# Optimization experiments

Hardware: AMD Instinct MI355X
Metric: run time of the kernel (lower is better)

Reference implementation:

```python
import jax, jax.numpy as jnp
import numpy as np

B, T, D, H = 4, 2048, 1024, 16
DH = D // H  # 64
EPS = 1e-5


def _layernorm(x, g, b):
    mu = jnp.mean(x, axis=-1, keepdims=True)
    var = jnp.var(x, axis=-1, keepdims=True)
    return (x - mu) * jax.lax.rsqrt(var + EPS) * g + b


def setup_inputs() -> dict:
    key = jax.random.key(0)
    ks = jax.random.split(key, 12)
    s = 0.02
    x = jax.random.normal(ks[0], (B, T, D), dtype=jnp.float32)
    # causal mask (the repo registers tril as the eos_mask buffer)
    eos_mask = jnp.broadcast_to(jnp.tril(jnp.ones((T, T), dtype=jnp.int32)), (B, T, T))
    Wq = jax.random.normal(ks[1], (H, D, DH), dtype=jnp.float32) * s
    Wk = jax.random.normal(ks[2], (H, D, DH), dtype=jnp.float32) * s
    Wv = jax.random.normal(ks[3], (H, D, DH), dtype=jnp.float32) * s
    Wp = jax.random.normal(ks[4], (D, D), dtype=jnp.float32) * s
    bp = jnp.zeros((D,), dtype=jnp.float32)
    W1 = jax.random.normal(ks[5], (D, 4 * D), dtype=jnp.float32) * s
    b1 = jnp.zeros((4 * D,), dtype=jnp.float32)
    W2 = jax.random.normal(ks[6], (4 * D, D), dtype=jnp.float32) * s
    b2 = jnp.zeros((D,), dtype=jnp.float32)
    g1 = jnp.ones((D,), dtype=jnp.float32)
    beta1 = jnp.zeros((D,), dtype=jnp.float32)
    g2 = jnp.ones((D,), dtype=jnp.float32)
    beta2 = jnp.zeros((D,), dtype=jnp.float32)
    return dict(x=x, eos_mask=eos_mask, Wq=Wq, Wk=Wk, Wv=Wv, Wp=Wp, bp=bp,
                W1=W1, b1=b1, W2=W2, b2=b2, g1=g1, beta1=beta1, g2=g2, beta2=beta2)


def reference(x, eos_mask, Wq, Wk, Wv, Wp, bp, W1, b1, W2, b2, g1, beta1, g2, beta2):
    # x: [B,T,D]; eos_mask: [B,T,T]
    x1 = _layernorm(x, g1, beta1)
    q = jnp.einsum('btd,hdk->bhtk', x1, Wq)
    k = jnp.einsum('btd,hdk->bhtk', x1, Wk)
    v = jnp.einsum('btd,hdk->bhtk', x1, Wv)
    # NOTE: original scales by 1/sqrt(C) where C = d_model (not d_head)
    scores = jnp.einsum('bhtk,bhsk->bhts', q, k) / np.sqrt(x.shape[-1]).astype(np.float32)
    scores = jnp.where(eos_mask[:, None, :, :] == 0, jnp.float32(-jnp.inf), scores)
    wei = jax.nn.softmax(scores, axis=-1)
    attn = jnp.einsum('bhts,bhsk->bhtk', wei, v)          # [B,H,T,DH]
    attn = attn.transpose(0, 2, 1, 3).reshape(x.shape)    # concat heads -> [B,T,D]
    attn = attn @ Wp + bp
    x2 = x1 + attn
    x3 = _layernorm(x2, g2, beta2)
    mlp = jax.nn.relu(x3 @ W1 + b1) @ W2 + b2
    out = x3 + mlp
    return out
```

## Files before the change

kernel.cpp:

```cpp
#include <hip/hip_runtime.h>


#define B_ 4
#define T_ 2048
#define D_ 1024
#define H_ 16
#define DH_ 64

using u16 = unsigned short;
typedef short bf16x8 __attribute__((ext_vector_type(8)));
typedef float f32x4 __attribute__((ext_vector_type(4)));

#define GLOAD_LDS16(g, l)                                                          \
  __builtin_amdgcn_global_load_lds((const __attribute__((address_space(1))) void*)(g), \
                                   (__attribute__((address_space(3))) void*)(l), 16, 0, 0)

#define CVTPK(d, lo, hi) asm("v_cvt_pk_bf16_f32 %0, %1, %2" : "=v"(d) : "v"(lo), "v"(hi))
#define BARSB() do { __builtin_amdgcn_s_barrier(); __builtin_amdgcn_sched_barrier(0); } while (0)

__device__ __forceinline__ f32x4 mfma16(bf16x8 a, bf16x8 b, f32x4 c) {
  return __builtin_amdgcn_mfma_f32_16x16x32_bf16(a, b, c, 0, 0, 0);
}

__device__ __forceinline__ u16 f2bf(float f) {
  union { float f; unsigned u; } v; v.f = f;
  unsigned r = v.u + 0x7fffu + ((v.u >> 16) & 1u);
  return (u16)(r >> 16);
}
__device__ __forceinline__ float bf2f(u16 h) {
  union { unsigned u; float f; } v; v.u = ((unsigned)h) << 16; return v.f;
}

template<typename TI>
__global__ __launch_bounds__(256)
void ln_kernel(const TI* __restrict__ x, const float* __restrict__ g,
               const float* __restrict__ be, u16* __restrict__ yb)
{
  const int row = blockIdx.x;
  const int tid = threadIdx.x;
  float v0, v1, v2, v3;
  if constexpr (sizeof(TI) == 4) {
    const float4 vx = ((const float4*)(x + (size_t)row * D_))[tid];
    v0 = vx.x; v1 = vx.y; v2 = vx.z; v3 = vx.w;
  } else {
    const ushort4 vx = ((const ushort4*)((const u16*)x + (size_t)row * D_))[tid];
    v0 = bf2f(vx.x); v1 = bf2f(vx.y); v2 = bf2f(vx.z); v3 = bf2f(vx.w);
  }
  float s  = v0 + v1 + v2 + v3;
  float s2 = v0*v0 + v1*v1 + v2*v2 + v3*v3;
#pragma unroll
  for (int m = 1; m < 64; m <<= 1) { s += __shfl_xor(s, m); s2 += __shfl_xor(s2, m); }
  __shared__ float red[8];
  const int w = tid >> 6;
  if ((tid & 63) == 0) { red[w] = s; red[4 + w] = s2; }
  __syncthreads();
  s  = red[0] + red[1] + red[2] + red[3];
  s2 = red[4] + red[5] + red[6] + red[7];
  const float mu   = s * (1.0f / D_);
  const float rstd = rsqrtf(s2 * (1.0f / D_) - mu * mu + 1e-5f);
  const float4 gg = ((const float4*)g)[tid];
  const float4 bb = ((const float4*)be)[tid];
  ushort4 pk;
  pk.x = f2bf((v0 - mu) * rstd * gg.x + bb.x);
  pk.y = f2bf((v1 - mu) * rstd * gg.y + bb.y);
  pk.z = f2bf((v2 - mu) * rstd * gg.z + bb.z);
  pk.w = f2bf((v3 - mu) * rstd * gg.w + bb.w);
  ((ushort4*)(yb + (size_t)row * D_))[tid] = pk;
}

__global__ __launch_bounds__(256)
void transpose_cvt(const float* __restrict__ in, u16* __restrict__ out, int R, int C)
{
  __shared__ float tile[32][33];
  const int c0 = blockIdx.x * 32, r0 = blockIdx.y * 32;
  const float* ip = in + (size_t)blockIdx.z * R * C;
  u16* op = out + (size_t)blockIdx.z * R * C;
  const int tx = threadIdx.x, ty = threadIdx.y;
#pragma unroll
  for (int j = 0; j < 4; ++j)
    tile[ty + j * 8][tx] = ip[(size_t)(r0 + ty + j * 8) * C + (c0 + tx)];
  __syncthreads();
#pragma unroll
  for (int j = 0; j < 4; ++j)
    op[(size_t)(c0 + ty + j * 8) * R + (r0 + tx)] = f2bf(tile[tx][ty + j * 8]);
}

__global__ __launch_bounds__(256)
void transpose_bf(const u16* __restrict__ in, u16* __restrict__ out, int R, int C)
{
  __shared__ u16 tile[32][34];
  const int c0 = blockIdx.x * 32, r0 = blockIdx.y * 32;
  const u16* ip = in + (size_t)blockIdx.z * R * C;
  u16* op = out + (size_t)blockIdx.z * R * C;
  const int tx = threadIdx.x, ty = threadIdx.y;
#pragma unroll
  for (int j = 0; j < 4; ++j)
    tile[ty + j * 8][tx] = ip[(size_t)(r0 + ty + j * 8) * C + (c0 + tx)];
  __syncthreads();
#pragma unroll
  for (int j = 0; j < 4; ++j)
    op[(size_t)(c0 + ty + j * 8) * R + (r0 + tx)] = tile[tx][ty + j * 8];
}

#define MODE_QKV 0
#define MODE_WP 1
#define MODE_MLP1 2
#define MODE_MLP2 3

template<int MODE>
__global__ __launch_bounds__(512, 2)
void gemm256v3(const u16* __restrict__ A, const u16* __restrict__ Bt,
               int M, int N, int K,
               const float* __restrict__ bias, const u16* __restrict__ resid,
               float* __restrict__ outf, u16* __restrict__ outb,
               u16* __restrict__ qo, u16* __restrict__ ko, u16* __restrict__ vo)
{
  __shared__ __align__(16) u16 Ash[2][256 * 64];
  __shared__ __align__(16) u16 Bsh[2][256 * 64];
  const int t = threadIdx.x, w = t >> 6, l = t & 63, lg = l >> 4, lr = l & 15;
  const int wr = w >> 2, wc = w & 3;

  const int gx = gridDim.x;
  const int nwg = gx * gridDim.y;
  const int bid = blockIdx.y * gx + blockIdx.x;
  const int cpx = nwg >> 3;
  const int virt = (bid & 7) * cpx + (bid >> 3);
  const int bn0 = (virt % gx) * 256, bm0 = (virt / gx) * 256;

  f32x4 acc[8][4] = {};

  const int srow = t >> 3;
  const int sc16 = (t & 7) ^ (srow & 7);
  const u16* gAs = A  + (size_t)(bm0 + srow) * K + sc16 * 8;
  const u16* gBs = Bt + (size_t)(bn0 + srow) * K + sc16 * 8;

#define ISS2_A(R, BUF, ko) GLOAD_LDS16(gAs + (size_t)(R) * 64 * K + (ko), &Ash[BUF][(R) * 4096 + w * 512])
#define ISS2_B(R, BUF, ko) GLOAD_LDS16(gBs + (size_t)(R) * 64 * K + (ko), &Bsh[BUF][(R) * 4096 + w * 512])

  const int nkt = K >> 6;
  ISS2_A(0, 0, 0); ISS2_A(1, 0, 0); ISS2_A(2, 0, 0); ISS2_A(3, 0, 0);
  ISS2_B(0, 0, 0); ISS2_B(1, 0, 0); ISS2_B(2, 0, 0); ISS2_B(3, 0, 0);
  if (nkt > 1) {
    ISS2_A(0, 1, 64); ISS2_A(2, 1, 64);
    asm volatile("s_waitcnt vmcnt(2)" ::: "memory");
  } else {
    asm volatile("s_waitcnt vmcnt(0)" ::: "memory");
  }
  BARSB();

  auto rdA0k = [&](int buf, int m) -> bf16x8 {
    const int r = wr * 128 + m * 16 + lr;
    return *(const bf16x8*)((const char*)&Ash[buf][0] + r * 128 + (((0 + lg) ^ (r & 7)) << 4));
  };
  auto rdA1k = [&](int buf, int m) -> bf16x8 {
    const int r = wr * 128 + m * 16 + lr;
    return *(const bf16x8*)((const char*)&Ash[buf][0] + r * 128 + (((4 + lg) ^ (r & 7)) << 4));
  };
  auto rdB0k = [&](int buf, int n) -> bf16x8 {
    const int r = wc * 64 + n * 16 + lr;
    return *(const bf16x8*)((const char*)&Bsh[buf][0] + r * 128 + (((0 + lg) ^ (r & 7)) << 4));
  };
  auto rdB1k = [&](int buf, int n) -> bf16x8 {
    const int r = wc * 64 + n * 16 + lr;
    return *(const bf16x8*)((const char*)&Bsh[buf][0] + r * 128 + (((4 + lg) ^ (r & 7)) << 4));
  };

  bf16x8 afr[4][2], bfr[4][2];

  for (int i = 0; i < nkt; ++i) {
    const int buf = i & 1, nb = buf ^ 1;
    const size_t k1 = (size_t)(i + 1) << 6, k2 = (size_t)(i + 2) << 6;
    const bool n1 = (i + 1 < nkt), n2 = (i + 2 < nkt);

#pragma unroll
    for (int m = 0; m < 4; ++m) { afr[m][0] = rdA0k(buf, m); afr[m][1] = rdA1k(buf, m); }
#pragma unroll
    for (int n = 0; n < 4; ++n) { bfr[n][0] = rdB0k(buf, n); bfr[n][1] = rdB1k(buf, n); }
    if (n1) { ISS2_A(1, nb, k1); ISS2_A(3, nb, k1); ISS2_B(2, nb, k1); ISS2_B(3, nb, k1); }
    __builtin_amdgcn_s_setprio(1);
#pragma unroll
    for (int m = 0; m < 4; ++m)
#pragma unroll
      for (int n = 0; n < 4; ++n) {
        acc[m][n] = mfma16(afr[m][0], bfr[n][0], acc[m][n]);
        acc[m][n] = mfma16(afr[m][1], bfr[n][1], acc[m][n]);
      }
    __builtin_amdgcn_s_setprio(0);
    BARSB();

#pragma unroll
    for (int m = 0; m < 4; ++m) { afr[m][0] = rdA0k(buf, 4 + m); afr[m][1] = rdA1k(buf, 4 + m); }
    if (n1) { ISS2_B(0, nb, k1); ISS2_B(1, nb, k1); }
    if (n2) { ISS2_A(0, buf, k2); ISS2_A(2, buf, k2); }
    __builtin_amdgcn_s_setprio(1);
#pragma unroll
    for (int m = 0; m < 4; ++m)
#pragma unroll
      for (int n = 0; n < 4; ++n) {
        acc[4 + m][n] = mfma16(afr[m][0], bfr[n][0], acc[4 + m][n]);
        acc[4 + m][n] = mfma16(afr[m][1], bfr[n][1], acc[4 + m][n]);
      }
    __builtin_amdgcn_s_setprio(0);
    if (n1) {
      if (n2) asm volatile("s_waitcnt vmcnt(2)" ::: "memory");
      else    asm volatile("s_waitcnt vmcnt(0)" ::: "memory");
      BARSB();
    }
  }
#undef ISS2_A
#undef ISS2_B

#pragma unroll
  for (int m = 0; m < 8; ++m) {
#pragma unroll
    for (int n = 0; n < 4; ++n) {
#pragma unroll
      for (int r = 0; r < 4; ++r) {
        const int row = bm0 + wr * 128 + m * 16 + lg * 4 + r;
        const int col = bn0 + wc * 64 + n * 16 + lr;
        float v = acc[m][n][r];
        if constexpr (MODE == MODE_QKV) {
          const int sel = col >> 10, hh = (col >> 6) & 15, dh = col & 63;
          const int bi = row >> 11, tt = row & 2047;
          u16* dst = (sel == 0) ? qo : (sel == 1) ? ko : vo;
          dst[(((size_t)bi * H_ + hh) * T_ + tt) * DH_ + dh] = f2bf(v);
        } else if constexpr (MODE == MODE_MLP1) {
          v += bias[col];
          outb[(size_t)row * N + col] = f2bf(v > 0.f ? v : 0.f);
        }
      }
    }
  }
}

template<int MODE>
__global__ __launch_bounds__(512, 4)
void gemm128(const u16* __restrict__ A, const u16* __restrict__ Bt,
             int M, int N, int K,
             const float* __restrict__ bias, const u16* __restrict__ resid,
             float* __restrict__ outf, u16* __restrict__ outb,
             u16* __restrict__ qo, u16* __restrict__ ko, u16* __restrict__ vo)
{
  __shared__ __align__(16) u16 Ash[2][128 * 64];
  __shared__ __align__(16) u16 Bsh[2][128 * 64];
  const int t = threadIdx.x, w = t >> 6, l = t & 63, lg = l >> 4, lr = l & 15;
  const int wr = w >> 2, wc = w & 3;

  const int gx = gridDim.x;
  const int nwg = gx * gridDim.y;
  const int bid = blockIdx.y * gx + blockIdx.x;
  const int cpx = nwg >> 3;
  const int virt = (bid & 7) * cpx + (bid >> 3);
  const int bn0 = (virt % gx) * 128, bm0 = (virt / gx) * 128;

  f32x4 acc[4][2] = {};

  const int srow = t >> 3;
  const int sc16 = (t & 7) ^ (srow & 7);
  const u16* gAs = A  + (size_t)(bm0 + srow) * K + sc16 * 8;
  const u16* gBs = Bt + (size_t)(bn0 + srow) * K + sc16 * 8;

#define ISS_A(R, BUF, ko) GLOAD_LDS16(gAs + (size_t)(R) * 64 * K + (ko), &Ash[BUF][(R) * 4096 + w * 512])
#define ISS_B(R, BUF, ko) GLOAD_LDS16(gBs + (size_t)(R) * 64 * K + (ko), &Bsh[BUF][(R) * 4096 + w * 512])

  ISS_A(0, 0, 0); ISS_A(1, 0, 0); ISS_B(0, 0, 0); ISS_B(1, 0, 0);
  ISS_A(0, 1, 64); ISS_A(1, 1, 64); ISS_B(0, 1, 64); ISS_B(1, 1, 64);

  auto rdA = [&](int buf, int m, int kk) -> bf16x8 {
    const int r = wr * 64 + m * 16 + lr;
    return *(const bf16x8*)((const char*)&Ash[buf][0] + r * 128 + (((kk * 4 + lg) ^ (r & 7)) << 4));
  };
  auto rdB = [&](int buf, int n, int kk) -> bf16x8 {
    const int r = wc * 32 + n * 16 + lr;
    return *(const bf16x8*)((const char*)&Bsh[buf][0] + r * 128 + (((kk * 4 + lg) ^ (r & 7)) << 4));
  };

  const int nkt = K >> 6;
  for (int i = 0; i < nkt; ++i) {
    const int buf = i & 1;
    if (i + 1 < nkt) asm volatile("s_waitcnt vmcnt(4)" ::: "memory");
    else             asm volatile("s_waitcnt vmcnt(0)" ::: "memory");
    BARSB();

    bf16x8 afr[4][2], bfr[2][2];
#pragma unroll
    for (int m = 0; m < 4; ++m) { afr[m][0] = rdA(buf, m, 0); afr[m][1] = rdA(buf, m, 1); }
#pragma unroll
    for (int n = 0; n < 2; ++n) { bfr[n][0] = rdB(buf, n, 0); bfr[n][1] = rdB(buf, n, 1); }

    __builtin_amdgcn_s_setprio(1);
#pragma unroll
    for (int m = 0; m < 4; ++m)
#pragma unroll
      for (int n = 0; n < 2; ++n) {
        acc[m][n] = mfma16(afr[m][0], bfr[n][0], acc[m][n]);
        acc[m][n] = mfma16(afr[m][1], bfr[n][1], acc[m][n]);
      }
    __builtin_amdgcn_s_setprio(0);
    BARSB();

    if (i + 2 < nkt) {
      const size_t ko = (size_t)(i + 2) << 6;
      ISS_A(0, buf, ko); ISS_A(1, buf, ko); ISS_B(0, buf, ko); ISS_B(1, buf, ko);
    }
  }
#undef ISS_A
#undef ISS_B

#pragma unroll
  for (int m = 0; m < 4; ++m) {
#pragma unroll
    for (int n = 0; n < 2; ++n) {
#pragma unroll
      for (int r = 0; r < 4; ++r) {
        const int row = bm0 + wr * 64 + m * 16 + lg * 4 + r;
        const int col = bn0 + wc * 32 + n * 16 + lr;
        float v = acc[m][n][r];
        if constexpr (MODE == MODE_WP) {
          v += bias[col] + bf2f(resid[(size_t)row * N + col]);
          outb[(size_t)row * N + col] = f2bf(v);
        } else if constexpr (MODE == MODE_MLP2) {
          outf[(size_t)row * N + col] = v + bias[col] + bf2f(resid[(size_t)row * N + col]);
        }
      }
    }
  }
}

__global__ __launch_bounds__(512, 4)
void attn_kernel(const u16* __restrict__ q, const u16* __restrict__ k,
                 const u16* __restrict__ vt, u16* __restrict__ out)
{
  __shared__ __align__(16) u16 Ks[2][4096];
  __shared__ __align__(16) u16 Vs[2][4096];
  const int t = threadIdx.x, w = t >> 6, l = t & 63, lg = l >> 4, lr = l & 15;

  const int bid = blockIdx.x;
  const int xcd = bid & 7, v = bid >> 3;
  const int bh = xcd * 8 + (v & 7);
  const int pair = v >> 3;

  const int b = bh >> 4, h = bh & 15;
  const u16* Qp  = q  + (size_t)bh * T_ * DH_;
  const u16* Kp  = k  + (size_t)bh * T_ * DH_;
  const u16* Vtp = vt + (size_t)bh * T_ * DH_;

  const int srow = t >> 3;
  const int schunk = ((t & 7) ^ (srow & 7)) << 3;
  const u16* Kg = Kp  + (size_t)srow * DH_ + schunk;
  const u16* Vg = Vtp + (size_t)srow * T_  + schunk;

  const float SC2 = 0.03125f * 1.44269504f;
  const float THR2 = 11.5416f;
  const size_t obase = ((size_t)b * T_) * D_ + (size_t)h * DH_;

#pragma unroll 1
  for (int pass = 0; pass < 2; ++pass) {
    const int qt = pass == 0 ? (15 - pair) : pair;
    const int qrow = qt * 128 + w * 16 + lr;
    const bf16x8 qf0 = *(const bf16x8*)&Qp[(size_t)qrow * DH_ + lg * 8];
    const bf16x8 qf1 = *(const bf16x8*)&Qp[(size_t)qrow * DH_ + 32 + lg * 8];

    float m_run = -1e30f, l_run = 0.f;
    f32x4 o[4] = {};

    GLOAD_LDS16(Kg, &Ks[0][w * 512]);
    GLOAD_LDS16(Vg, &Vs[0][w * 512]);
    __syncthreads();

    const int nst = 2 * qt + 2;
    for (int st = 0; st < nst; ++st) {
      const int cur = st & 1, nxt = cur ^ 1;
      const bool pf = (st + 1 < nst);
      if (pf) {
        GLOAD_LDS16(Kg + (size_t)(st + 1) * 64 * DH_, &Ks[nxt][w * 512]);
        GLOAD_LDS16(Vg + (size_t)(st + 1) * 64,       &Vs[nxt][w * 512]);
      }

      f32x4 sa[4] = {};
      const char* kb = (const char*)&Ks[cur][0];
      __builtin_amdgcn_s_setprio(1);
#pragma unroll
      for (int n = 0; n < 4; ++n) {
        const int sr = n * 16 + lr;
        const int base = (sr << 7) + (lg << 4);
        const int swz = (sr & 7) << 4;
        const bf16x8 b0 = *(const bf16x8*)(kb + (base ^ swz));
        const bf16x8 b1 = *(const bf16x8*)(kb + ((base + 64) ^ swz));
        sa[n] = mfma16(b0, qf0, sa[n]);
        sa[n] = mfma16(b1, qf1, sa[n]);
      }
      __builtin_amdgcn_s_setprio(0);

      float sc[4][4];
      float rm = -1e30f;
#pragma unroll
      for (int n = 0; n < 4; ++n)
#pragma unroll
        for (int r = 0; r < 4; ++r)
          sc[n][r] = sa[n][r] * SC2;
      if (st >= 2 * qt) {
#pragma unroll
        for (int n = 0; n < 4; ++n)
#pragma unroll
          for (int r = 0; r < 4; ++r)
            if (st * 64 + n * 16 + lg * 4 + r > qrow) sc[n][r] = -1e30f;
      }
#pragma unroll
      for (int n = 0; n < 4; ++n)
#pragma unroll
        for (int r = 0; r < 4; ++r)
          rm = fmaxf(rm, sc[n][r]);
      rm = fmaxf(rm, __shfl_xor(rm, 16));
      rm = fmaxf(rm, __shfl_xor(rm, 32));
      const bool noresc = __all(rm <= m_run + THR2);
      if (!noresc) {
        const float mnew = fmaxf(m_run, rm);
        const float al = exp2f(m_run - mnew);
        m_run = mnew;
        l_run *= al;
        const float alr0 = __shfl(al, lg * 4 + 0);
        const float alr1 = __shfl(al, lg * 4 + 1);
        const float alr2 = __shfl(al, lg * 4 + 2);
        const float alr3 = __shfl(al, lg * 4 + 3);
#pragma unroll
        for (int n = 0; n < 4; ++n) {
          o[n][0] *= alr0; o[n][1] *= alr1; o[n][2] *= alr2; o[n][3] *= alr3;
        }
      }
      float rs = 0.f;
#pragma unroll
      for (int n = 0; n < 4; ++n)
#pragma unroll
        for (int r = 0; r < 4; ++r) {
          sc[n][r] = exp2f(sc[n][r] - m_run);
          rs += sc[n][r];
        }
      rs += __shfl_xor(rs, 16);
      rs += __shfl_xor(rs, 32);
      l_run += rs;

      unsigned pk0a, pk0b, pk1a, pk1b, pk2a, pk2b, pk3a, pk3b;
      CVTPK(pk0a, sc[0][0], sc[0][1]); CVTPK(pk0b, sc[0][2], sc[0][3]);
      CVTPK(pk1a, sc[1][0], sc[1][1]); CVTPK(pk1b, sc[1][2], sc[1][3]);
      CVTPK(pk2a, sc[2][0], sc[2][1]); CVTPK(pk2b, sc[2][2], sc[2][3]);
      CVTPK(pk3a, sc[3][0], sc[3][1]); CVTPK(pk3b, sc[3][2], sc[3][3]);

      const int srcA = lr + ((l >> 4) & 1) * 32;
      const int srcB = srcA + 16;
      const bool hi = (l >> 5) & 1;
      union { uint4 u; bf16x8 v8; } f0, f1;
      {
        const unsigned xA0 = __shfl(pk0a, srcA), xA1 = __shfl(pk0b, srcA);
        const unsigned yA0 = __shfl(pk1a, srcA), yA1 = __shfl(pk1b, srcA);
        const unsigned xB0 = __shfl(pk0a, srcB), xB1 = __shfl(pk0b, srcB);
        const unsigned yB0 = __shfl(pk1a, srcB), yB1 = __shfl(pk1b, srcB);
        f0.u.x = hi ? yA0 : xA0; f0.u.y = hi ? yA1 : xA1;
        f0.u.z = hi ? yB0 : xB0; f0.u.w = hi ? yB1 : xB1;
      }
      {
        const unsigned xA0 = __shfl(pk2a, srcA), xA1 = __shfl(pk2b, srcA);
        const unsigned yA0 = __shfl(pk3a, srcA), yA1 = __shfl(pk3b, srcA);
        const unsigned xB0 = __shfl(pk2a, srcB), xB1 = __shfl(pk2b, srcB);
        const unsigned yB0 = __shfl(pk3a, srcB), yB1 = __shfl(pk3b, srcB);
        f1.u.x = hi ? yA0 : xA0; f1.u.y = hi ? yA1 : xA1;
        f1.u.z = hi ? yB0 : xB0; f1.u.w = hi ? yB1 : xB1;
      }

      const char* vbase = (const char*)&Vs[cur][0];
      __builtin_amdgcn_s_setprio(1);
#pragma unroll
      for (int ks = 0; ks < 2; ++ks) {
        const bf16x8 pa = ks ? f1.v8 : f0.v8;
#pragma unroll
        for (int n = 0; n < 4; ++n) {
          const int dh = n * 16 + lr;
          const int base = (dh << 7) + (ks << 6) + (lg << 4);
          const int swz = (dh & 7) << 4;
          const bf16x8 vbf = *(const bf16x8*)(vbase + (base ^ swz));
          o[n] = mfma16(pa, vbf, o[n]);
        }
      }
      __builtin_amdgcn_s_setprio(0);

      __syncthreads();
    }

    float li[4];
    li[0] = 1.0f / __shfl(l_run, lg * 4 + 0);
    li[1] = 1.0f / __shfl(l_run, lg * 4 + 1);
    li[2] = 1.0f / __shfl(l_run, lg * 4 + 2);
    li[3] = 1.0f / __shfl(l_run, lg * 4 + 3);
#pragma unroll
    for (int n = 0; n < 4; ++n) {
#pragma unroll
      for (int r = 0; r < 4; ++r) {
        const int qg = qt * 128 + w * 16 + lg * 4 + r;
        out[obase + (size_t)qg * D_ + n * 16 + lr] = f2bf(o[n][r] * li[r]);
      }
    }
    __syncthreads();
  }
}

extern "C" void kernel_launch(void* const* d_in, const int* in_sizes, int n_in,
                              void* d_out, int out_size, void* d_ws, size_t ws_size,
                              hipStream_t stream) {
  (void)in_sizes; (void)n_in; (void)out_size; (void)ws_size;
  const float* x   = (const float*)d_in[0];
  const float* Wq  = (const float*)d_in[2];
  const float* Wk  = (const float*)d_in[3];
  const float* Wv  = (const float*)d_in[4];
  const float* Wp  = (const float*)d_in[5];
  const float* bp  = (const float*)d_in[6];
  const float* W1  = (const float*)d_in[7];
  const float* b1  = (const float*)d_in[8];
  const float* W2  = (const float*)d_in[9];
  const float* b2  = (const float*)d_in[10];
  const float* g1  = (const float*)d_in[11];
  const float* be1 = (const float*)d_in[12];
  const float* g2  = (const float*)d_in[13];
  const float* be2 = (const float*)d_in[14];

  char* ws = (char*)d_ws;
  const size_t MB16 = 16777216;
  u16* x1b   = (u16*)(ws);
  u16* qb    = (u16*)(ws + 1 * MB16);
  u16* kb    = (u16*)(ws + 2 * MB16);
  u16* vb    = (u16*)(ws + 3 * MB16);
  u16* attnb = (u16*)(ws + 4 * MB16);
  u16* x2b   = (u16*)(ws + 5 * MB16);
  u16* hb    = (u16*)(ws + 6 * MB16);
  u16* vtb   = hb;
  u16* wqkvb = (u16*)(ws + 10 * MB16);
  u16* wpb   = (u16*)(ws + 10 * MB16 + 6291456);
  u16* w1b   = (u16*)(ws + 10 * MB16 + 8388608);
  u16* w2b   = (u16*)(ws + 11 * MB16);
  u16* x3b   = qb;

  dim3 tb(32, 8, 1);
  transpose_cvt<<<dim3(2, 32, 16),  tb, 0, stream>>>(Wq, wqkvb,                    1024, 64);
  transpose_cvt<<<dim3(2, 32, 16),  tb, 0, stream>>>(Wk, wqkvb + (size_t)1048576,  1024, 64);
  transpose_cvt<<<dim3(2, 32, 16),  tb, 0, stream>>>(Wv, wqkvb + (size_t)2097152,  1024, 64);
  transpose_cvt<<<dim3(32, 32, 1),  tb, 0, stream>>>(Wp, wpb, 1024, 1024);
  transpose_cvt<<<dim3(128, 32, 1), tb, 0, stream>>>(W1, w1b, 1024, 4096);
  transpose_cvt<<<dim3(32, 128, 1), tb, 0, stream>>>(W2, w2b, 4096, 1024);

  ln_kernel<float><<<8192, 256, 0, stream>>>(x, g1, be1, x1b);

  gemm256v3<MODE_QKV><<<dim3(12, 32), 512, 0, stream>>>(
      x1b, wqkvb, 8192, 3072, 1024, nullptr, nullptr, nullptr, nullptr, qb, kb, vb);

  transpose_bf<<<dim3(2, 64, 64), tb, 0, stream>>>(vb, vtb, 2048, 64);

  attn_kernel<<<dim3(512), 512, 0, stream>>>(qb, kb, vtb, attnb);

  gemm128<MODE_WP><<<dim3(8, 64), 512, 0, stream>>>(
      attnb, wpb, 8192, 1024, 1024, bp, x1b, nullptr, x2b, nullptr, nullptr, nullptr);

  ln_kernel<u16><<<8192, 256, 0, stream>>>(x2b, g2, be2, x3b);

  gemm256v3<MODE_MLP1><<<dim3(16, 32), 512, 0, stream>>>(
      x3b, w1b, 8192, 4096, 1024, b1, nullptr, nullptr, hb, nullptr, nullptr, nullptr);

  gemm128<MODE_MLP2><<<dim3(8, 64), 512, 0, stream>>>(
      hb, w2b, 8192, 1024, 4096, b2, x3b, (float*)d_out, nullptr, nullptr, nullptr, nullptr);
}
```

Measured before the change: 362.8 us.

## Widen attention KV tile to 128, prescale Q, merge QKV weight transposes

The attention kernel now processes 128-key tiles per step instead of 64, halving loop iterations and barriers, with doubled LDS buffers and a new V swizzle layout. The softmax scale is folded into Q once per pass, so the per-score multiply is gone. Separately, the three QKV weight transpose launches are merged into one, and the GEMM issues all B-tile prefetches in the first half of each k-step. Larger tiles raise LDS use and register pressure. Prescaling Q in bf16 adds a rounding step.

Result: faster. 354.7 us (-2.2%).

```diff
diff --git a/kernel.cpp b/kernel.cpp
--- a/kernel.cpp
+++ b/kernel.cpp
@@ -86,6 +86,27 @@
 }
 
 __global__ __launch_bounds__(256)
+void transpose_cvt3(const float* __restrict__ w0, const float* __restrict__ w1,
+                    const float* __restrict__ w2, u16* __restrict__ out)
+{
+  __shared__ float tile[32][33];
+  const int R = 1024, C = 64;
+  const int mat = blockIdx.z >> 4, zz = blockIdx.z & 15;
+  const float* in = (mat == 0) ? w0 : (mat == 1) ? w1 : w2;
+  const int c0 = blockIdx.x * 32, r0 = blockIdx.y * 32;
+  const float* ip = in + (size_t)zz * R * C;
+  u16* op = out + (size_t)mat * 1048576 + (size_t)zz * R * C;
+  const int tx = threadIdx.x, ty = threadIdx.y;
+#pragma unroll
+  for (int j = 0; j < 4; ++j)
+    tile[ty + j * 8][tx] = ip[(size_t)(r0 + ty + j * 8) * C + (c0 + tx)];
+  __syncthreads();
+#pragma unroll
+  for (int j = 0; j < 4; ++j)
+    op[(size_t)(c0 + ty + j * 8) * R + (r0 + tx)] = f2bf(tile[tx][ty + j * 8]);
+}
+
+__global__ __launch_bounds__(256)
 void transpose_bf(const u16* __restrict__ in, u16* __restrict__ out, int R, int C)
 {
   __shared__ u16 tile[32][34];
@@ -176,7 +197,10 @@
     for (int m = 0; m < 4; ++m) { afr[m][0] = rdA0k(buf, m); afr[m][1] = rdA1k(buf, m); }
 #pragma unroll
     for (int n = 0; n < 4; ++n) { bfr[n][0] = rdB0k(buf, n); bfr[n][1] = rdB1k(buf, n); }
-    if (n1) { ISS2_A(1, nb, k1); ISS2_A(3, nb, k1); ISS2_B(2, nb, k1); ISS2_B(3, nb, k1); }
+    if (n1) {
+      ISS2_A(1, nb, k1); ISS2_A(3, nb, k1);
+      ISS2_B(0, nb, k1); ISS2_B(1, nb, k1); ISS2_B(2, nb, k1); ISS2_B(3, nb, k1);
+    }
     __builtin_amdgcn_s_setprio(1);
 #pragma unroll
     for (int m = 0; m < 4; ++m)
@@ -190,7 +214,6 @@
 
 #pragma unroll
     for (int m = 0; m < 4; ++m) { afr[m][0] = rdA0k(buf, 4 + m); afr[m][1] = rdA1k(buf, 4 + m); }
-    if (n1) { ISS2_B(0, nb, k1); ISS2_B(1, nb, k1); }
     if (n2) { ISS2_A(0, buf, k2); ISS2_A(2, buf, k2); }
     __builtin_amdgcn_s_setprio(1);
 #pragma unroll
@@ -331,24 +354,26 @@
 void attn_kernel(const u16* __restrict__ q, const u16* __restrict__ k,
                  const u16* __restrict__ vt, u16* __restrict__ out)
 {
-  __shared__ __align__(16) u16 Ks[2][4096];
-  __shared__ __align__(16) u16 Vs[2][4096];
+  __shared__ __align__(16) u16 Ks[2][8192];
+  __shared__ __align__(16) u16 Vs[2][8192];
   const int t = threadIdx.x, w = t >> 6, l = t & 63, lg = l >> 4, lr = l & 15;
 
   const int bid = blockIdx.x;
-  const int xcd = bid & 7, v = bid >> 3;
-  const int bh = xcd * 8 + (v & 7);
-  const int pair = v >> 3;
+  const int xcd = bid & 7, vv = bid >> 3;
+  const int bh = xcd * 8 + (vv & 7);
+  const int pair = vv >> 3;
 
   const int b = bh >> 4, h = bh & 15;
   const u16* Qp  = q  + (size_t)bh * T_ * DH_;
   const u16* Kp  = k  + (size_t)bh * T_ * DH_;
   const u16* Vtp = vt + (size_t)bh * T_ * DH_;
 
-  const int srow = t >> 3;
-  const int schunk = ((t & 7) ^ (srow & 7)) << 3;
-  const u16* Kg = Kp  + (size_t)srow * DH_ + schunk;
-  const u16* Vg = Vtp + (size_t)srow * T_  + schunk;
+  const int srowK = t >> 3;
+  const int kchunk = ((t & 7) ^ (srowK & 7)) << 3;
+  const u16* Kg = Kp + (size_t)srowK * DH_ + kchunk;
+  const int srowV = t >> 4;
+  const int vchunk = ((t & 15) ^ (srowV & 7)) << 3;
+  const u16* Vg = Vtp + (size_t)srowV * T_ + vchunk;
 
   const float SC2 = 0.03125f * 1.44269504f;
   const float THR2 = 11.5416f;
@@ -358,30 +383,47 @@
   for (int pass = 0; pass < 2; ++pass) {
     const int qt = pass == 0 ? (15 - pair) : pair;
     const int qrow = qt * 128 + w * 16 + lr;
-    const bf16x8 qf0 = *(const bf16x8*)&Qp[(size_t)qrow * DH_ + lg * 8];
-    const bf16x8 qf1 = *(const bf16x8*)&Qp[(size_t)qrow * DH_ + 32 + lg * 8];
+    bf16x8 qf0 = *(const bf16x8*)&Qp[(size_t)qrow * DH_ + lg * 8];
+    bf16x8 qf1 = *(const bf16x8*)&Qp[(size_t)qrow * DH_ + 32 + lg * 8];
+    {
+      union { bf16x8 v8; u16 u[8]; unsigned wd[4]; } a0, a1, r0, r1;
+      a0.v8 = qf0; a1.v8 = qf1;
+#pragma unroll
+      for (int j = 0; j < 4; ++j) {
+        unsigned pk;
+        float lo = bf2f(a0.u[2 * j]) * SC2, hi = bf2f(a0.u[2 * j + 1]) * SC2;
+        CVTPK(pk, lo, hi); r0.wd[j] = pk;
+        lo = bf2f(a1.u[2 * j]) * SC2; hi = bf2f(a1.u[2 * j + 1]) * SC2;
+        CVTPK(pk, lo, hi); r1.wd[j] = pk;
+      }
+      qf0 = r0.v8; qf1 = r1.v8;
+    }
 
     float m_run = -1e30f, l_run = 0.f;
     f32x4 o[4] = {};
 
-    GLOAD_LDS16(Kg, &Ks[0][w * 512]);
-    GLOAD_LDS16(Vg, &Vs[0][w * 512]);
+    GLOAD_LDS16(Kg,            &Ks[0][w * 512]);
+    GLOAD_LDS16(Kg + 64 * DH_, &Ks[0][4096 + w * 512]);
+    GLOAD_LDS16(Vg,            &Vs[0][w * 512]);
+    GLOAD_LDS16(Vg + 32 * T_,  &Vs[0][4096 + w * 512]);
     __syncthreads();
 
-    const int nst = 2 * qt + 2;
+    const int nst = qt + 1;
     for (int st = 0; st < nst; ++st) {
       const int cur = st & 1, nxt = cur ^ 1;
-      const bool pf = (st + 1 < nst);
-      if (pf) {
-        GLOAD_LDS16(Kg + (size_t)(st + 1) * 64 * DH_, &Ks[nxt][w * 512]);
-        GLOAD_LDS16(Vg + (size_t)(st + 1) * 64,       &Vs[nxt][w * 512]);
-      }
-
-      f32x4 sa[4] = {};
+      if (st + 1 < nst) {
+        const size_t koff = (size_t)(st + 1) * 128 * DH_;
+        GLOAD_LDS16(Kg + koff,            &Ks[nxt][w * 512]);
+        GLOAD_LDS16(Kg + koff + 64 * DH_, &Ks[nxt][4096 + w * 512]);
+        GLOAD_LDS16(Vg + (st + 1) * 128,           &Vs[nxt][w * 512]);
+        GLOAD_LDS16(Vg + 32 * T_ + (st + 1) * 128, &Vs[nxt][4096 + w * 512]);
+      }
+
+      f32x4 sa[8] = {};
       const char* kb = (const char*)&Ks[cur][0];
       __builtin_amdgcn_s_setprio(1);
 #pragma unroll
-      for (int n = 0; n < 4; ++n) {
+      for (int n = 0; n < 8; ++n) {
         const int sr = n * 16 + lr;
         const int base = (sr << 7) + (lg << 4);
         const int swz = (sr & 7) << 4;
@@ -392,25 +434,19 @@
       }
       __builtin_amdgcn_s_setprio(0);
 
-      float sc[4][4];
+      if (st == qt) {
+#pragma unroll
+        for (int n = 0; n < 8; ++n)
+#pragma unroll
+          for (int r = 0; r < 4; ++r)
+            if (st * 128 + n * 16 + lg * 4 + r > qrow) sa[n][r] = -1e30f;
+      }
       float rm = -1e30f;
 #pragma unroll
-      for (int n = 0; n < 4; ++n)
+      for (int n = 0; n < 8; ++n)
 #pragma unroll
         for (int r = 0; r < 4; ++r)
-          sc[n][r] = sa[n][r] * SC2;
-      if (st >= 2 * qt) {
-#pragma unroll
-        for (int n = 0; n < 4; ++n)
-#pragma unroll
-          for (int r = 0; r < 4; ++r)
-            if (st * 64 + n * 16 + lg * 4 + r > qrow) sc[n][r] = -1e30f;
-      }
-#pragma unroll
-      for (int n = 0; n < 4; ++n)
-#pragma unroll
-        for (int r = 0; r < 4; ++r)
-          rm = fmaxf(rm, sc[n][r]);
+          rm = fmaxf(rm, sa[n][r]);
       rm = fmaxf(rm, __shfl_xor(rm, 16));
       rm = fmaxf(rm, __shfl_xor(rm, 32));
       const bool noresc = __all(rm <= m_run + THR2);
@@ -430,58 +466,47 @@
       }
       float rs = 0.f;
 #pragma unroll
-      for (int n = 0; n < 4; ++n)
+      for (int n = 0; n < 8; ++n)
 #pragma unroll
         for (int r = 0; r < 4; ++r) {
-          sc[n][r] = exp2f(sc[n][r] - m_run);
-          rs += sc[n][r];
+          sa[n][r] = exp2f(sa[n][r] - m_run);
+          rs += sa[n][r];
         }
       rs += __shfl_xor(rs, 16);
       rs += __shfl_xor(rs, 32);
       l_run += rs;
 
-      unsigned pk0a, pk0b, pk1a, pk1b, pk2a, pk2b, pk3a, pk3b;
-      CVTPK(pk0a, sc[0][0], sc[0][1]); CVTPK(pk0b, sc[0][2], sc[0][3]);
-      CVTPK(pk1a, sc[1][0], sc[1][1]); CVTPK(pk1b, sc[1][2], sc[1][3]);
-      CVTPK(pk2a, sc[2][0], sc[2][1]); CVTPK(pk2b, sc[2][2], sc[2][3]);
-      CVTPK(pk3a, sc[3][0], sc[3][1]); CVTPK(pk3b, sc[3][2], sc[3][3]);
-
-      const int srcA = lr + ((l >> 4) & 1) * 32;
+      unsigned pka[8], pkb[8];
+#pragma unroll
+      for (int n = 0; n < 8; ++n) {
+        unsigned x, y;
+        CVTPK(x, sa[n][0], sa[n][1]); CVTPK(y, sa[n][2], sa[n][3]);
+        pka[n] = x; pkb[n] = y;
+      }
+
+      const char* vbase = (const char*)&Vs[cur][0];
+      const int srcA = lr + (lg & 1) * 32;
       const int srcB = srcA + 16;
-      const bool hi = (l >> 5) & 1;
-      union { uint4 u; bf16x8 v8; } f0, f1;
-      {
-        const unsigned xA0 = __shfl(pk0a, srcA), xA1 = __shfl(pk0b, srcA);
-        const unsigned yA0 = __shfl(pk1a, srcA), yA1 = __shfl(pk1b, srcA);
-        const unsigned xB0 = __shfl(pk0a, srcB), xB1 = __shfl(pk0b, srcB);
-        const unsigned yB0 = __shfl(pk1a, srcB), yB1 = __shfl(pk1b, srcB);
-        f0.u.x = hi ? yA0 : xA0; f0.u.y = hi ? yA1 : xA1;
-        f0.u.z = hi ? yB0 : xB0; f0.u.w = hi ? yB1 : xB1;
-      }
-      {
-        const unsigned xA0 = __shfl(pk2a, srcA), xA1 = __shfl(pk2b, srcA);
-        const unsigned yA0 = __shfl(pk3a, srcA), yA1 = __shfl(pk3b, srcA);
-        const unsigned xB0 = __shfl(pk2a, srcB), xB1 = __shfl(pk2b, srcB);
-        const unsigned yB0 = __shfl(pk3a, srcB), yB1 = __shfl(pk3b, srcB);
-        f1.u.x = hi ? yA0 : xA0; f1.u.y = hi ? yA1 : xA1;
-        f1.u.z = hi ? yB0 : xB0; f1.u.w = hi ? yB1 : xB1;
-      }
-
-      const char* vbase = (const char*)&Vs[cur][0];
-      __builtin_amdgcn_s_setprio(1);
-#pragma unroll
-      for (int ks = 0; ks < 2; ++ks) {
-        const bf16x8 pa = ks ? f1.v8 : f0.v8;
+      const bool hi = (lg >> 1) & 1;
+#pragma unroll
+      for (int ks = 0; ks < 4; ++ks) {
+        union { uint4 u; bf16x8 v8; } f;
+        const unsigned xA0 = __shfl(pka[2 * ks],     srcA), xA1 = __shfl(pkb[2 * ks],     srcA);
+        const unsigned yA0 = __shfl(pka[2 * ks + 1], srcA), yA1 = __shfl(pkb[2 * ks + 1], srcA);
+        const unsigned xB0 = __shfl(pka[2 * ks],     srcB), xB1 = __shfl(pkb[2 * ks],     srcB);
+        const unsigned yB0 = __shfl(pka[2 * ks + 1], srcB), yB1 = __shfl(pkb[2 * ks + 1], srcB);
+        f.u.x = hi ? yA0 : xA0; f.u.y = hi ? yA1 : xA1;
+        f.u.z = hi ? yB0 : xB0; f.u.w = hi ? yB1 : xB1;
+        __builtin_amdgcn_s_setprio(1);
 #pragma unroll
         for (int n = 0; n < 4; ++n) {
           const int dh = n * 16 + lr;
-          const int base = (dh << 7) + (ks << 6) + (lg << 4);
-          const int swz = (dh & 7) << 4;
-          const bf16x8 vbf = *(const bf16x8*)(vbase + (base ^ swz));
-          o[n] = mfma16(pa, vbf, o[n]);
+          const int byte = dh * 256 + (((ks * 4 + lg) ^ (dh & 7)) << 4);
+          const bf16x8 vbf = *(const bf16x8*)(vbase + byte);
+          o[n] = mfma16(f.v8, vbf, o[n]);
         }
-      }
-      __builtin_amdgcn_s_setprio(0);
+        __builtin_amdgcn_s_setprio(0);
+      }
 
       __syncthreads();
     }
@@ -539,9 +564,7 @@
   u16* x3b   = qb;
 
   dim3 tb(32, 8, 1);
-  transpose_cvt<<<dim3(2, 32, 16),  tb, 0, stream>>>(Wq, wqkvb,                    1024, 64);
-  transpose_cvt<<<dim3(2, 32, 16),  tb, 0, stream>>>(Wk, wqkvb + (size_t)1048576,  1024, 64);
-  transpose_cvt<<<dim3(2, 32, 16),  tb, 0, stream>>>(Wv, wqkvb + (size_t)2097152,  1024, 64);
+  transpose_cvt3<<<dim3(2, 32, 48),  tb, 0, stream>>>(Wq, Wk, Wv, wqkvb);
   transpose_cvt<<<dim3(32, 32, 1),  tb, 0, stream>>>(Wp, wpb, 1024, 1024);
   transpose_cvt<<<dim3(128, 32, 1), tb, 0, stream>>>(W1, w1b, 1024, 4096);
   transpose_cvt<<<dim3(32, 128, 1), tb, 0, stream>>>(W2, w2b, 4096, 1024);
```

## Unify GEMMs on templated 256xBR tile kernel, fold Q scaling, merge QKV weight transposes

Applied to the files above, without the earlier changes.

Makes the 256-row GEMM kernel templated on the B-tile width, so the Wp and MLP2 GEMMs use 256x128 tiles instead of the separate 128x128 kernel. All B-tile loads now issue in the first half of each k-iteration. The attention kernel pre-scales Q by the softmax constant once, removing a per-element multiply on every score tile. The three QKV weight transposes are merged into one launch. Larger tiles raise register and LDS use and leave fewer workgroups for the N=1024 GEMMs, and rounding the scaled Q to bf16 slightly changes numerics.

Measured after the change: 356.8 us. No clear change (-1.7%).

```diff
diff --git a/kernel.cpp b/kernel.cpp
--- a/kernel.cpp
+++ b/kernel.cpp
@@ -86,6 +86,27 @@
 }
 
 __global__ __launch_bounds__(256)
+void transpose_cvt3(const float* __restrict__ w0, const float* __restrict__ w1,
+                    const float* __restrict__ w2, u16* __restrict__ out)
+{
+  __shared__ float tile[32][33];
+  const int R = 1024, C = 64;
+  const int mat = blockIdx.z >> 4, zz = blockIdx.z & 15;
+  const float* in = (mat == 0) ? w0 : (mat == 1) ? w1 : w2;
+  const int c0 = blockIdx.x * 32, r0 = blockIdx.y * 32;
+  const float* ip = in + (size_t)zz * R * C;
+  u16* op = out + (size_t)mat * 1048576 + (size_t)zz * R * C;
+  const int tx = threadIdx.x, ty = threadIdx.y;
+#pragma unroll
+  for (int j = 0; j < 4; ++j)
+    tile[ty + j * 8][tx] = ip[(size_t)(r0 + ty + j * 8) * C + (c0 + tx)];
+  __syncthreads();
+#pragma unroll
+  for (int j = 0; j < 4; ++j)
+    op[(size_t)(c0 + ty + j * 8) * R + (r0 + tx)] = f2bf(tile[tx][ty + j * 8]);
+}
+
+__global__ __launch_bounds__(256)
 void transpose_bf(const u16* __restrict__ in, u16* __restrict__ out, int R, int C)
 {
   __shared__ u16 tile[32][34];
@@ -107,7 +128,7 @@
 #define MODE_MLP1 2
 #define MODE_MLP2 3
 
-template<int MODE>
+template<int MODE, int BR>
 __global__ __launch_bounds__(512, 2)
 void gemm256v3(const u16* __restrict__ A, const u16* __restrict__ Bt,
                int M, int N, int K,
@@ -116,7 +137,7 @@
                u16* __restrict__ qo, u16* __restrict__ ko, u16* __restrict__ vo)
 {
   __shared__ __align__(16) u16 Ash[2][256 * 64];
-  __shared__ __align__(16) u16 Bsh[2][256 * 64];
+  __shared__ __align__(16) u16 Bsh[2][BR * 64 * 64];
   const int t = threadIdx.x, w = t >> 6, l = t & 63, lg = l >> 4, lr = l & 15;
   const int wr = w >> 2, wc = w & 3;
 
@@ -125,9 +146,9 @@
   const int bid = blockIdx.y * gx + blockIdx.x;
   const int cpx = nwg >> 3;
   const int virt = (bid & 7) * cpx + (bid >> 3);
-  const int bn0 = (virt % gx) * 256, bm0 = (virt / gx) * 256;
-
-  f32x4 acc[8][4] = {};
+  const int bn0 = (virt % gx) * (BR * 64), bm0 = (virt / gx) * 256;
+
+  f32x4 acc[8][BR] = {};
 
   const int srow = t >> 3;
   const int sc16 = (t & 7) ^ (srow & 7);
@@ -139,7 +160,8 @@
 
   const int nkt = K >> 6;
   ISS2_A(0, 0, 0); ISS2_A(1, 0, 0); ISS2_A(2, 0, 0); ISS2_A(3, 0, 0);
-  ISS2_B(0, 0, 0); ISS2_B(1, 0, 0); ISS2_B(2, 0, 0); ISS2_B(3, 0, 0);
+#pragma unroll
+  for (int r = 0; r < BR; ++r) ISS2_B(r, 0, 0);
   if (nkt > 1) {
     ISS2_A(0, 1, 64); ISS2_A(2, 1, 64);
     asm volatile("s_waitcnt vmcnt(2)" ::: "memory");
@@ -157,15 +179,15 @@
     return *(const bf16x8*)((const char*)&Ash[buf][0] + r * 128 + (((4 + lg) ^ (r & 7)) << 4));
   };
   auto rdB0k = [&](int buf, int n) -> bf16x8 {
-    const int r = wc * 64 + n * 16 + lr;
+    const int r = wc * (BR * 16) + n * 16 + lr;
     return *(const bf16x8*)((const char*)&Bsh[buf][0] + r * 128 + (((0 + lg) ^ (r & 7)) << 4));
   };
   auto rdB1k = [&](int buf, int n) -> bf16x8 {
-    const int r = wc * 64 + n * 16 + lr;
+    const int r = wc * (BR * 16) + n * 16 + lr;
     return *(const bf16x8*)((const char*)&Bsh[buf][0] + r * 128 + (((4 + lg) ^ (r & 7)) << 4));
   };
 
-  bf16x8 afr[4][2], bfr[4][2];
+  bf16x8 afr[4][2], bfr[BR][2];
 
   for (int i = 0; i < nkt; ++i) {
     const int buf = i & 1, nb = buf ^ 1;
@@ -175,13 +197,17 @@
 #pragma unroll
     for (int m = 0; m < 4; ++m) { afr[m][0] = rdA0k(buf, m); afr[m][1] = rdA1k(buf, m); }
 #pragma unroll
-    for (int n = 0; n < 4; ++n) { bfr[n][0] = rdB0k(buf, n); bfr[n][1] = rdB1k(buf, n); }
-    if (n1) { ISS2_A(1, nb, k1); ISS2_A(3, nb, k1); ISS2_B(2, nb, k1); ISS2_B(3, nb, k1); }
+    for (int n = 0; n < BR; ++n) { bfr[n][0] = rdB0k(buf, n); bfr[n][1] = rdB1k(buf, n); }
+    if (n1) {
+      ISS2_A(1, nb, k1); ISS2_A(3, nb, k1);
+#pragma unroll
+      for (int r = 0; r < BR; ++r) ISS2_B(r, nb, k1);
+    }
     __builtin_amdgcn_s_setprio(1);
 #pragma unroll
     for (int m = 0; m < 4; ++m)
 #pragma unroll
-      for (int n = 0; n < 4; ++n) {
+      for (int n = 0; n < BR; ++n) {
         acc[m][n] = mfma16(afr[m][0], bfr[n][0], acc[m][n]);
         acc[m][n] = mfma16(afr[m][1], bfr[n][1], acc[m][n]);
       }
@@ -190,13 +216,12 @@
 
 #pragma unroll
     for (int m = 0; m < 4; ++m) { afr[m][0] = rdA0k(buf, 4 + m); afr[m][1] = rdA1k(buf, 4 + m); }
-    if (n1) { ISS2_B(0, nb, k1); ISS2_B(1, nb, k1); }
     if (n2) { ISS2_A(0, buf, k2); ISS2_A(2, buf, k2); }
     __builtin_amdgcn_s_setprio(1);
 #pragma unroll
     for (int m = 0; m < 4; ++m)
 #pragma unroll
-      for (int n = 0; n < 4; ++n) {
+      for (int n = 0; n < BR; ++n) {
         acc[4 + m][n] = mfma16(afr[m][0], bfr[n][0], acc[4 + m][n]);
         acc[4 + m][n] = mfma16(afr[m][1], bfr[n][1], acc[4 + m][n]);
       }
@@ -213,11 +238,11 @@
 #pragma unroll
   for (int m = 0; m < 8; ++m) {
 #pragma unroll
-    for (int n = 0; n < 4; ++n) {
+    for (int n = 0; n < BR; ++n) {
 #pragma unroll
       for (int r = 0; r < 4; ++r) {
         const int row = bm0 + wr * 128 + m * 16 + lg * 4 + r;
-        const int col = bn0 + wc * 64 + n * 16 + lr;
+        const int col = bn0 + wc * (BR * 16) + n * 16 + lr;
         float v = acc[m][n][r];
         if constexpr (MODE == MODE_QKV) {
           const int sel = col >> 10, hh = (col >> 6) & 15, dh = col & 63;
@@ -227,96 +252,7 @@
         } else if constexpr (MODE == MODE_MLP1) {
           v += bias[col];
           outb[(size_t)row * N + col] = f2bf(v > 0.f ? v : 0.f);
-        }
-      }
-    }
-  }
-}
-
-template<int MODE>
-__global__ __launch_bounds__(512, 4)
-void gemm128(const u16* __restrict__ A, const u16* __restrict__ Bt,
-             int M, int N, int K,
-             const float* __restrict__ bias, const u16* __restrict__ resid,
-             float* __restrict__ outf, u16* __restrict__ outb,
-             u16* __restrict__ qo, u16* __restrict__ ko, u16* __restrict__ vo)
-{
-  __shared__ __align__(16) u16 Ash[2][128 * 64];
-  __shared__ __align__(16) u16 Bsh[2][128 * 64];
-  const int t = threadIdx.x, w = t >> 6, l = t & 63, lg = l >> 4, lr = l & 15;
-  const int wr = w >> 2, wc = w & 3;
-
-  const int gx = gridDim.x;
-  const int nwg = gx * gridDim.y;
-  const int bid = blockIdx.y * gx + blockIdx.x;
-  const int cpx = nwg >> 3;
-  const int virt = (bid & 7) * cpx + (bid >> 3);
-  const int bn0 = (virt % gx) * 128, bm0 = (virt / gx) * 128;
-
-  f32x4 acc[4][2] = {};
-
-  const int srow = t >> 3;
-  const int sc16 = (t & 7) ^ (srow & 7);
-  const u16* gAs = A  + (size_t)(bm0 + srow) * K + sc16 * 8;
-  const u16* gBs = Bt + (size_t)(bn0 + srow) * K + sc16 * 8;
-
-#define ISS_A(R, BUF, ko) GLOAD_LDS16(gAs + (size_t)(R) * 64 * K + (ko), &Ash[BUF][(R) * 4096 + w * 512])
-#define ISS_B(R, BUF, ko) GLOAD_LDS16(gBs + (size_t)(R) * 64 * K + (ko), &Bsh[BUF][(R) * 4096 + w * 512])
-
-  ISS_A(0, 0, 0); ISS_A(1, 0, 0); ISS_B(0, 0, 0); ISS_B(1, 0, 0);
-  ISS_A(0, 1, 64); ISS_A(1, 1, 64); ISS_B(0, 1, 64); ISS_B(1, 1, 64);
-
-  auto rdA = [&](int buf, int m, int kk) -> bf16x8 {
-    const int r = wr * 64 + m * 16 + lr;
-    return *(const bf16x8*)((const char*)&Ash[buf][0] + r * 128 + (((kk * 4 + lg) ^ (r & 7)) << 4));
-  };
-  auto rdB = [&](int buf, int n, int kk) -> bf16x8 {
-    const int r = wc * 32 + n * 16 + lr;
-    return *(const bf16x8*)((const char*)&Bsh[buf][0] + r * 128 + (((kk * 4 + lg) ^ (r & 7)) << 4));
-  };
-
-  const int nkt = K >> 6;
-  for (int i = 0; i < nkt; ++i) {
-    const int buf = i & 1;
-    if (i + 1 < nkt) asm volatile("s_waitcnt vmcnt(4)" ::: "memory");
-    else             asm volatile("s_waitcnt vmcnt(0)" ::: "memory");
-    BARSB();
-
-    bf16x8 afr[4][2], bfr[2][2];
-#pragma unroll
-    for (int m = 0; m < 4; ++m) { afr[m][0] = rdA(buf, m, 0); afr[m][1] = rdA(buf, m, 1); }
-#pragma unroll
-    for (int n = 0; n < 2; ++n) { bfr[n][0] = rdB(buf, n, 0); bfr[n][1] = rdB(buf, n, 1); }
-
-    __builtin_amdgcn_s_setprio(1);
-#pragma unroll
-    for (int m = 0; m < 4; ++m)
-#pragma unroll
-      for (int n = 0; n < 2; ++n) {
-        acc[m][n] = mfma16(afr[m][0], bfr[n][0], acc[m][n]);
-        acc[m][n] = mfma16(afr[m][1], bfr[n][1], acc[m][n]);
-      }
-    __builtin_amdgcn_s_setprio(0);
-    BARSB();
-
-    if (i + 2 < nkt) {
-      const size_t ko = (size_t)(i + 2) << 6;
-      ISS_A(0, buf, ko); ISS_A(1, buf, ko); ISS_B(0, buf, ko); ISS_B(1, buf, ko);
-    }
-  }
-#undef ISS_A
-#undef ISS_B
-
-#pragma unroll
-  for (int m = 0; m < 4; ++m) {
-#pragma unroll
-    for (int n = 0; n < 2; ++n) {
-#pragma unroll
-      for (int r = 0; r < 4; ++r) {
-        const int row = bm0 + wr * 64 + m * 16 + lg * 4 + r;
-        const int col = bn0 + wc * 32 + n * 16 + lr;
-        float v = acc[m][n][r];
-        if constexpr (MODE == MODE_WP) {
+        } else if constexpr (MODE == MODE_WP) {
           v += bias[col] + bf2f(resid[(size_t)row * N + col]);
           outb[(size_t)row * N + col] = f2bf(v);
         } else if constexpr (MODE == MODE_MLP2) {
@@ -336,9 +272,9 @@
   const int t = threadIdx.x, w = t >> 6, l = t & 63, lg = l >> 4, lr = l & 15;
 
   const int bid = blockIdx.x;
-  const int xcd = bid & 7, v = bid >> 3;
-  const int bh = xcd * 8 + (v & 7);
-  const int pair = v >> 3;
+  const int xcd = bid & 7, vv = bid >> 3;
+  const int bh = xcd * 8 + (vv & 7);
+  const int pair = vv >> 3;
 
   const int b = bh >> 4, h = bh & 15;
   const u16* Qp  = q  + (size_t)bh * T_ * DH_;
@@ -358,8 +294,21 @@
   for (int pass = 0; pass < 2; ++pass) {
     const int qt = pass == 0 ? (15 - pair) : pair;
     const int qrow = qt * 128 + w * 16 + lr;
-    const bf16x8 qf0 = *(const bf16x8*)&Qp[(size_t)qrow * DH_ + lg * 8];
-    const bf16x8 qf1 = *(const bf16x8*)&Qp[(size_t)qrow * DH_ + 32 + lg * 8];
+    bf16x8 qf0 = *(const bf16x8*)&Qp[(size_t)qrow * DH_ + lg * 8];
+    bf16x8 qf1 = *(const bf16x8*)&Qp[(size_t)qrow * DH_ + 32 + lg * 8];
+    {
+      union { bf16x8 v8; u16 u[8]; unsigned wd[4]; } a0, a1, r0, r1;
+      a0.v8 = qf0; a1.v8 = qf1;
+#pragma unroll
+      for (int j = 0; j < 4; ++j) {
+        unsigned pk;
+        float lo = bf2f(a0.u[2 * j]) * SC2, hi = bf2f(a0.u[2 * j + 1]) * SC2;
+        CVTPK(pk, lo, hi); r0.wd[j] = pk;
+        lo = bf2f(a1.u[2 * j]) * SC2; hi = bf2f(a1.u[2 * j + 1]) * SC2;
+        CVTPK(pk, lo, hi); r1.wd[j] = pk;
+      }
+      qf0 = r0.v8; qf1 = r1.v8;
+    }
 
     float m_run = -1e30f, l_run = 0.f;
     f32x4 o[4] = {};
@@ -392,25 +341,19 @@
       }
       __builtin_amdgcn_s_setprio(0);
 
-      float sc[4][4];
+      if (st >= 2 * qt) {
+#pragma unroll
+        for (int n = 0; n < 4; ++n)
+#pragma unroll
+          for (int r = 0; r < 4; ++r)
+            if (st * 64 + n * 16 + lg * 4 + r > qrow) sa[n][r] = -1e30f;
+      }
       float rm = -1e30f;
 #pragma unroll
       for (int n = 0; n < 4; ++n)
 #pragma unroll
         for (int r = 0; r < 4; ++r)
-          sc[n][r] = sa[n][r] * SC2;
-      if (st >= 2 * qt) {
-#pragma unroll
-        for (int n = 0; n < 4; ++n)
-#pragma unroll
-          for (int r = 0; r < 4; ++r)
-            if (st * 64 + n * 16 + lg * 4 + r > qrow) sc[n][r] = -1e30f;
-      }
-#pragma unroll
-      for (int n = 0; n < 4; ++n)
-#pragma unroll
-        for (int r = 0; r < 4; ++r)
-          rm = fmaxf(rm, sc[n][r]);
+          rm = fmaxf(rm, sa[n][r]);
       rm = fmaxf(rm, __shfl_xor(rm, 16));
       rm = fmaxf(rm, __shfl_xor(rm, 32));
       const bool noresc = __all(rm <= m_run + THR2);
@@ -433,18 +376,18 @@
       for (int n = 0; n < 4; ++n)
 #pragma unroll
         for (int r = 0; r < 4; ++r) {
-          sc[n][r] = exp2f(sc[n][r] - m_run);
-          rs += sc[n][r];
+          sa[n][r] = exp2f(sa[n][r] - m_run);
+          rs += sa[n][r];
         }
       rs += __shfl_xor(rs, 16);
       rs += __shfl_xor(rs, 32);
       l_run += rs;
 
       unsigned pk0a, pk0b, pk1a, pk1b, pk2a, pk2b, pk3a, pk3b;
-      CVTPK(pk0a, sc[0][0], sc[0][1]); CVTPK(pk0b, sc[0][2], sc[0][3]);
-      CVTPK(pk1a, sc[1][0], sc[1][1]); CVTPK(pk1b, sc[1][2], sc[1][3]);
-      CVTPK(pk2a, sc[2][0], sc[2][1]); CVTPK(pk2b, sc[2][2], sc[2][3]);
-      CVTPK(pk3a, sc[3][0], sc[3][1]); CVTPK(pk3b, sc[3][2], sc[3][3]);
+      CVTPK(pk0a, sa[0][0], sa[0][1]); CVTPK(pk0b, sa[0][2], sa[0][3]);
+      CVTPK(pk1a, sa[1][0], sa[1][1]); CVTPK(pk1b, sa[1][2], sa[1][3]);
+      CVTPK(pk2a, sa[2][0], sa[2][1]); CVTPK(pk2b, sa[2][2], sa[2][3]);
+      CVTPK(pk3a, sa[3][0], sa[3][1]); CVTPK(pk3b, sa[3][2], sa[3][3]);
 
       const int srcA = lr + ((l >> 4) & 1) * 32;
       const int srcB = srcA + 16;
@@ -539,30 +482,28 @@
   u16* x3b   = qb;
 
   dim3 tb(32, 8, 1);
-  transpose_cvt<<<dim3(2, 32, 16),  tb, 0, stream>>>(Wq, wqkvb,                    1024, 64);
-  transpose_cvt<<<dim3(2, 32, 16),  tb, 0, stream>>>(Wk, wqkvb + (size_t)1048576,  1024, 64);
-  transpose_cvt<<<dim3(2, 32, 16),  tb, 0, stream>>>(Wv, wqkvb + (size_t)2097152,  1024, 64);
+  transpose_cvt3<<<dim3(2, 32, 48),  tb, 0, stream>>>(Wq, Wk, Wv, wqkvb);
   transpose_cvt<<<dim3(32, 32, 1),  tb, 0, stream>>>(Wp, wpb, 1024, 1024);
   transpose_cvt<<<dim3(128, 32, 1), tb, 0, stream>>>(W1, w1b, 1024, 4096);
   transpose_cvt<<<dim3(32, 128, 1), tb, 0, stream>>>(W2, w2b, 4096, 1024);
 
   ln_kernel<float><<<8192, 256, 0, stream>>>(x, g1, be1, x1b);
 
-  gemm256v3<MODE_QKV><<<dim3(12, 32), 512, 0, stream>>>(
+  gemm256v3<MODE_QKV, 4><<<dim3(12, 32), 512, 0, stream>>>(
       x1b, wqkvb, 8192, 3072, 1024, nullptr, nullptr, nullptr, nullptr, qb, kb, vb);
 
   transpose_bf<<<dim3(2, 64, 64), tb, 0, stream>>>(vb, vtb, 2048, 64);
 
   attn_kernel<<<dim3(512), 512, 0, stream>>>(qb, kb, vtb, attnb);
 
-  gemm128<MODE_WP><<<dim3(8, 64), 512, 0, stream>>>(
+  gemm256v3<MODE_WP, 2><<<dim3(8, 32), 512, 0, stream>>>(
       attnb, wpb, 8192, 1024, 1024, bp, x1b, nullptr, x2b, nullptr, nullptr, nullptr);
 
   ln_kernel<u16><<<8192, 256, 0, stream>>>(x2b, g2, be2, x3b);
 
-  gemm256v3<MODE_MLP1><<<dim3(16, 32), 512, 0, stream>>>(
+  gemm256v3<MODE_MLP1, 4><<<dim3(16, 32), 512, 0, stream>>>(
       x3b, w1b, 8192, 4096, 1024, b1, nullptr, nullptr, hb, nullptr, nullptr, nullptr);
 
-  gemm128<MODE_MLP2><<<dim3(8, 64), 512, 0, stream>>>(
+  gemm256v3<MODE_MLP2, 2><<<dim3(8, 32), 512, 0, stream>>>(
       hb, w2b, 8192, 1024, 4096, b2, x3b, (float*)d_out, nullptr, nullptr, nullptr, nullptr);
 }
```
